# Kernel tuning notes

Measured on AMD Instinct MI355X. Metric: run time of the kernel, lower is better.

## Reference

```python
import jax, jax.numpy as jnp
import numpy as np

EMBED_DIM = 1024
NUM_HEADS = 16
HEAD_DIM = EMBED_DIM // NUM_HEADS
SCALE = HEAD_DIM ** -0.5


def setup_inputs() -> dict:
    key = jax.random.key(0)
    ks = jax.random.split(key, 7)
    B, S, D = 4, 2048, EMBED_DIM
    return {
        "x": jax.random.normal(ks[0], (B, S, D), dtype=jnp.float32),
        "gamma": jnp.ones((D,), dtype=jnp.float32),
        "beta": jnp.zeros((D,), dtype=jnp.float32),
        "w_qkv": jax.random.normal(ks[1], (D, 3 * D), dtype=jnp.float32) * (D ** -0.5),
        "b_qkv": jax.random.normal(ks[2], (3 * D,), dtype=jnp.float32) * 0.02,
        "w_proj": jax.random.normal(ks[3], (D, D), dtype=jnp.float32) * (D ** -0.5),
        "b_proj": jax.random.normal(ks[4], (D,), dtype=jnp.float32) * 0.02,
    }


def reference(x, gamma, beta, w_qkv, b_qkv, w_proj, b_proj):
    B, S, D = x.shape
    # pre-norm LayerNorm (eps=1e-5, torch default)
    mu = jnp.mean(x, axis=-1, keepdims=True)
    var = jnp.mean(jnp.square(x - mu), axis=-1, keepdims=True)
    xn = (x - mu) * jax.lax.rsqrt(var + 1e-5) * gamma + beta
    # fused QKV projection -> (3, B, H, S, hd)
    qkv = (xn @ w_qkv + b_qkv).reshape(B, S, 3, NUM_HEADS, HEAD_DIM)
    qkv = jnp.transpose(qkv, (2, 0, 3, 1, 4))
    q, k, v = qkv[0], qkv[1], qkv[2]
    scores = jnp.einsum("bhqd,bhkd->bhqk", q, k) * SCALE
    attn = jax.nn.softmax(scores, axis=-1)  # dropout p=0 -> no-op
    ctx = jnp.einsum("bhqk,bhkd->bhqd", attn, v)
    ctx = jnp.transpose(ctx, (0, 2, 1, 3)).reshape(B, S, D)
    return ctx @ w_proj + b_proj
```

## Files before the change

kernel.cpp:

```cpp
#include <hip/hip_runtime.h>

typedef unsigned short ushort_t;
typedef __attribute__((ext_vector_type(8))) short bf16x8;
typedef __attribute__((ext_vector_type(4))) float f32x4;
typedef __attribute__((ext_vector_type(16))) float f32x16;
typedef __attribute__((ext_vector_type(2))) __bf16 bf16v2;

#define BN 4
#define SEQ 2048
#define DIM 1024
#define NH 16
#define HDIM 64
#define MROWS (BN*SEQ)
#define QSCALE 0.18033688011112042f

__device__ __forceinline__ float bf2f(ushort_t s){ return __uint_as_float(((unsigned)s) << 16); }
__device__ __forceinline__ ushort_t f2bf(float f){
  unsigned u = __float_as_uint(f);
  u += 0x7fffu + ((u >> 16) & 1u);
  return (ushort_t)(u >> 16);
}
__device__ __forceinline__ unsigned pack2(float a, float b){
  return (unsigned)f2bf(a) | ((unsigned)f2bf(b) << 16);
}

__global__ __launch_bounds__(256) void ln_kernel(const float* __restrict__ x,
                                                 const float* __restrict__ gamma,
                                                 const float* __restrict__ beta,
                                                 ushort_t* __restrict__ xnb)
{
  int row = blockIdx.x;
  int t = threadIdx.x;
  float4 v = ((const float4*)(x + (size_t)row * DIM))[t];
  float s = v.x+v.y+v.z+v.w;
  float ss = v.x*v.x+v.y*v.y+v.z*v.z+v.w*v.w;
  #pragma unroll
  for (int o = 32; o > 0; o >>= 1){ s += __shfl_down(s, o); ss += __shfl_down(ss, o); }
  __shared__ float red[10];
  int wid = t >> 6;
  if ((t & 63) == 0){ red[wid] = s; red[4+wid] = ss; }
  __syncthreads();
  if (t == 0){
    float S0 = red[0]+red[1]+red[2]+red[3];
    float SS = red[4]+red[5]+red[6]+red[7];
    float mu = S0 * (1.f/DIM);
    float var = SS * (1.f/DIM) - mu*mu;
    red[8] = mu; red[9] = rsqrtf(var + 1e-5f);
  }
  __syncthreads();
  float mu = red[8], rstd = red[9];
  float4 g = ((const float4*)gamma)[t];
  float4 b = ((const float4*)beta)[t];
  float f0 = (v.x - mu)*rstd*g.x + b.x;
  float f1 = (v.y - mu)*rstd*g.y + b.y;
  float f2 = (v.z - mu)*rstd*g.z + b.z;
  float f3 = (v.w - mu)*rstd*g.w + b.w;
  *(uint2*)(xnb + (size_t)row*DIM + t*4) = make_uint2(pack2(f0,f1), pack2(f2,f3));
}

__global__ __launch_bounds__(256) void cvt_t(const float* __restrict__ src,
                                             ushort_t* __restrict__ dst,
                                             int K, int N, float qscale)
{
  __shared__ float tile[64][65];
  int k0 = blockIdx.y*64, n0 = blockIdx.x*64;
  float sc = (n0 < 1024) ? qscale : 1.f;
  int t = threadIdx.x;
  int c = (t & 15) * 4, r = t >> 4;
  #pragma unroll
  for (int p = 0; p < 4; p++){
    float4 v = *(const float4*)(src + (size_t)(k0 + r + p*16)*N + n0 + c);
    tile[r+p*16][c]   = v.x; tile[r+p*16][c+1] = v.y;
    tile[r+p*16][c+2] = v.z; tile[r+p*16][c+3] = v.w;
  }
  __syncthreads();
  #pragma unroll
  for (int p = 0; p < 4; p++){
    int nn = r + p*16;
    ushort4 o;
    o.x = f2bf(tile[c+0][nn]*sc); o.y = f2bf(tile[c+1][nn]*sc);
    o.z = f2bf(tile[c+2][nn]*sc); o.w = f2bf(tile[c+3][nn]*sc);
    *(ushort4*)(dst + (size_t)(n0+nn)*K + k0 + c) = o;
  }
}

__global__ __launch_bounds__(256) void vtrans(const ushort_t* __restrict__ V,
                                              ushort_t* __restrict__ vt)
{
  __shared__ ushort_t tile[64][72];
  int bh = blockIdx.x >> 5, sc = blockIdx.x & 31;
  int t = threadIdx.x;
  const ushort_t* src = V + ((size_t)bh*SEQ + sc*64)*HDIM;
  #pragma unroll
  for (int p = 0; p < 2; p++){
    int idx = p*256 + t;
    int r = idx >> 3, c8 = (idx & 7)*8;
    *(uint4*)&tile[r][c8] = *(const uint4*)(src + (size_t)r*HDIM + c8);
  }
  __syncthreads();
  ushort_t* dstp = vt + ((size_t)(bh*32 + sc))*HDIM*64;
  #pragma unroll
  for (int p = 0; p < 2; p++){
    int idx = p*256 + t;
    int d = idx >> 3, c8 = (idx & 7)*8;
    uint4 u;
    u.x = (unsigned)tile[c8+0][d] | ((unsigned)tile[c8+1][d] << 16);
    u.y = (unsigned)tile[c8+2][d] | ((unsigned)tile[c8+3][d] << 16);
    u.z = (unsigned)tile[c8+4][d] | ((unsigned)tile[c8+5][d] << 16);
    u.w = (unsigned)tile[c8+6][d] | ((unsigned)tile[c8+7][d] << 16);
    *(uint4*)(dstp + (size_t)d*64 + c8) = u;
  }
}

template<int MODE, int NCOLS>
__global__ __launch_bounds__(256) void mfma_gemm(
    const ushort_t* __restrict__ A,
    const ushort_t* __restrict__ BT,
    const float* __restrict__ bias,
    void* __restrict__ Cv)
{
  __shared__ __align__(16) unsigned char smem[17408];
  ushort_t (*As)[128][8] = (ushort_t(*)[128][8])smem;
  ushort_t (*Bs)[128][8] = (ushort_t(*)[128][8])(smem + 8192);

  int t = threadIdx.x;
  int lane = t & 63, w = t >> 6;
  int col = lane & 15, quad = lane >> 4;
  int n0 = blockIdx.x * 128, m0 = blockIdx.y * 128;
  int sr = t >> 1, h = t & 1;

  f32x4 acc[4][4];
  #pragma unroll
  for (int i = 0; i < 4; i++)
    #pragma unroll
    for (int j = 0; j < 4; j++) acc[i][j] = (f32x4){0.f,0.f,0.f,0.f};

  int mbase = (w & 1)*64 + col;
  int nbase = (w >> 1)*64 + col;

  for (int k0 = 0; k0 < DIM; k0 += 32){
    const ushort_t* ap = A + (size_t)(m0 + sr)*DIM + k0 + h*16;
    uint4 aa0 = *(const uint4*)ap, aa1 = *(const uint4*)(ap + 8);
    const ushort_t* bp = BT + (size_t)(n0 + sr)*DIM + k0 + h*16;
    uint4 bb0 = *(const uint4*)bp, bb1 = *(const uint4*)(bp + 8);

    __syncthreads();
    *(uint4*)&As[2*h  ][sr][0] = aa0;
    *(uint4*)&As[2*h+1][sr][0] = aa1;
    *(uint4*)&Bs[2*h  ][sr][0] = bb0;
    *(uint4*)&Bs[2*h+1][sr][0] = bb1;
    __syncthreads();

    bf16x8 af[4], bfr[4];
    #pragma unroll
    for (int i = 0; i < 4; i++){
      af[i]  = *(const bf16x8*)&As[quad][mbase + i*16][0];
      bfr[i] = *(const bf16x8*)&Bs[quad][nbase + i*16][0];
    }
    #pragma unroll
    for (int mt = 0; mt < 4; mt++)
      #pragma unroll
      for (int nt = 0; nt < 4; nt++)
        acc[mt][nt] = __builtin_amdgcn_mfma_f32_16x16x32_bf16(af[mt], bfr[nt], acc[mt][nt], 0, 0, 0);
  }

  float bscale = (MODE == 2 && n0 < 1024) ? QSCALE : 1.f;
  float bv[4];
  #pragma unroll
  for (int nt = 0; nt < 4; nt++) bv[nt] = bias[n0 + (w>>1)*64 + nt*16 + col] * bscale;

  if (MODE == 2){
    ushort_t (*Cs)[136] = (ushort_t(*)[136])smem;
    ushort_t* C = (ushort_t*)Cv;
    #pragma unroll
    for (int ph = 0; ph < 2; ph++){
      __syncthreads();
      if ((w & 1) == ph){
        #pragma unroll
        for (int mt = 0; mt < 4; mt++)
          #pragma unroll
          for (int nt = 0; nt < 4; nt++)
            #pragma unroll
            for (int r = 0; r < 4; r++)
              Cs[mt*16 + quad*4 + r][(w>>1)*64 + nt*16 + col] = f2bf(acc[mt][nt][r] + bv[nt]);
      }
      __syncthreads();
      #pragma unroll
      for (int p = 0; p < 4; p++){
        int id = p*256 + t;
        int row = id >> 4, cc = id & 15;
        uint4 u = *(const uint4*)&Cs[row][cc*8];
        int m = m0 + ph*64 + row;
        int n = n0 + cc*8;
        int which = n >> 10, hh = (n >> 6) & 15, d = n & 63;
        int b_ = m >> 11, s_ = m & (SEQ-1);
        *(uint4*)&C[((((size_t)which*BN + b_)*NH + hh)*SEQ + s_)*HDIM + d] = u;
      }
    }
  } else {
    float (*Cf)[132] = (float(*)[132])smem;
    float* C = (float*)Cv;
    #pragma unroll
    for (int ph = 0; ph < 4; ph++){
      __syncthreads();
      if ((w & 1) == (ph >> 1)){
        #pragma unroll
        for (int mi = 0; mi < 2; mi++){
          int mt = (ph & 1)*2 + mi;
          #pragma unroll
          for (int nt = 0; nt < 4; nt++)
            #pragma unroll
            for (int r = 0; r < 4; r++)
              Cf[mi*16 + quad*4 + r][(w>>1)*64 + nt*16 + col] = acc[mt][nt][r] + bv[nt];
        }
      }
      __syncthreads();
      #pragma unroll
      for (int p = 0; p < 4; p++){
        int id = p*256 + t;
        int row = id >> 5, cc = id & 31;
        float4 v = *(const float4*)&Cf[row][cc*4];
        int m = m0 + ph*32 + row;
        *(float4*)(C + (size_t)m*NCOLS + n0 + cc*4) = v;
      }
    }
  }
}

__global__ __launch_bounds__(256) void attn_kernel(const ushort_t* __restrict__ qkv,
                                                   const ushort_t* __restrict__ vtp,
                                                   ushort_t* __restrict__ ctx)
{
  __shared__ __align__(16) unsigned char lds[36864];
  ushort_t (*Ks)[64][8] = (ushort_t(*)[64][8])lds;
  ushort_t (*Vs)[64][8] = (ushort_t(*)[64][8])(lds + 8192);

  int t = threadIdx.x;
  int lane = t & 63, w = t >> 6;
  int m32 = lane & 31, half = lane >> 5;
  int id = blockIdx.x;
  int bh = (id & 7) | ((id >> 7) << 3);
  int qb = (id >> 3) & 15;

  const size_t PL = (size_t)BN * NH * SEQ * HDIM;
  const ushort_t* Qg = qkv + (size_t)bh * (SEQ * HDIM);
  const ushort_t* Kg = Qg + PL;
  const ushort_t* Vt = vtp + (size_t)bh * 32 * (HDIM * 64);
  int qbase = qb*128 + w*32;

  bf16x8 qf[4];
  #pragma unroll
  for (int c = 0; c < 4; c++)
    qf[c] = *(const bf16x8*)(Qg + (size_t)(qbase + m32)*HDIM + c*16 + half*8);

  bf16x8 ones;
  #pragma unroll
  for (int i = 0; i < 8; i++) ones[i] = (short)0x3F80;

  f32x16 accO[2], accL;
  #pragma unroll
  for (int i = 0; i < 2; i++)
    #pragma unroll
    for (int r = 0; r < 16; r++) accO[i][r] = 0.f;
  #pragma unroll
  for (int r = 0; r < 16; r++) accL[r] = 0.f;

  int srow = t >> 2, sch = t & 3;
  const ushort_t* kp0 = Kg + (size_t)srow*HDIM + sch*16;
  const ushort_t* vp0 = Vt + (size_t)srow*64 + sch*16;

  uint4 kr0, kr1, vr0, vr1;
  kr0 = *(const uint4*)kp0;  kr1 = *(const uint4*)(kp0 + 8);
  vr0 = *(const uint4*)vp0;  vr1 = *(const uint4*)(vp0 + 8);

  for (int kt = 0; kt < 32; kt++){
    __syncthreads();
    *(uint4*)&Ks[sch*2  ][srow][0] = kr0;
    *(uint4*)&Ks[sch*2+1][srow][0] = kr1;
    *(uint4*)&Vs[sch*2  ][srow][0] = vr0;
    *(uint4*)&Vs[sch*2+1][srow][0] = vr1;
    __syncthreads();

    if (kt < 31){
      const ushort_t* kp = kp0 + (size_t)(kt+1)*64*HDIM;
      const ushort_t* vp = vp0 + (size_t)(kt+1)*HDIM*64;
      kr0 = *(const uint4*)kp;  kr1 = *(const uint4*)(kp + 8);
      vr0 = *(const uint4*)vp;  vr1 = *(const uint4*)(vp + 8);
    }

    bf16x8 pb[4];
    #pragma unroll
    for (int mt = 0; mt < 2; mt++){
      f32x16 z;
      #pragma unroll
      for (int r = 0; r < 16; r++) z[r] = 0.f;
      #pragma unroll
      for (int c = 0; c < 4; c++){
        bf16x8 af = *(const bf16x8*)&Ks[2*c + half][mt*32 + m32][0];
        z = __builtin_amdgcn_mfma_f32_32x32x16_bf16(af, qf[c], z, 0, 0, 0);
      }
      unsigned u[8];
      #pragma unroll
      for (int i = 0; i < 8; i++){
        float p0 = __builtin_amdgcn_exp2f(z[2*i]);
        float p1 = __builtin_amdgcn_exp2f(z[2*i+1]);
        bf16v2 hh; hh.x = (__bf16)p0; hh.y = (__bf16)p1;
        u[i] = __builtin_bit_cast(unsigned, hh);
      }
      #pragma unroll
      for (int cc = 0; cc < 2; cc++){
        union { uint4 q; bf16x8 b; } cvt;
        cvt.q = make_uint4(u[4*cc+0], u[4*cc+1], u[4*cc+2], u[4*cc+3]);
        pb[mt*2 + cc] = cvt.b;
      }
    }

    #pragma unroll
    for (int kc = 0; kc < 4; kc++)
      accL = __builtin_amdgcn_mfma_f32_32x32x16_bf16(ones, pb[kc], accL, 0, 0, 0);

    #pragma unroll
    for (int kc = 0; kc < 4; kc++){
      #pragma unroll
      for (int md = 0; md < 2; md++){
        int dd = md*32 + m32;
        union { bf16x8 v8; uint2 u2[2]; } vv;
        vv.u2[0] = *(const uint2*)&Vs[2*kc  ][dd][4*half];
        vv.u2[1] = *(const uint2*)&Vs[2*kc+1][dd][4*half];
        accO[md] = __builtin_amdgcn_mfma_f32_32x32x16_bf16(vv.v8, pb[kc], accO[md], 0, 0, 0);
      }
    }
  }

  float inv = 1.f / accL[0];

  ushort_t (*Os)[72] = (ushort_t(*)[72])(lds + 18432 + w*4608);
  #pragma unroll
  for (int md = 0; md < 2; md++)
    #pragma unroll
    for (int g = 0; g < 4; g++){
      int d0 = 8*g + 4*half + 32*md;
      unsigned lo = pack2(accO[md][4*g+0]*inv, accO[md][4*g+1]*inv);
      unsigned hi = pack2(accO[md][4*g+2]*inv, accO[md][4*g+3]*inv);
      *(uint2*)&Os[m32][d0] = make_uint2(lo, hi);
    }

  int b_ = bh >> 4, h_ = bh & 15;
  #pragma unroll
  for (int k = 0; k < 4; k++){
    int row = k*8 + (lane >> 3);
    uint4 u = *(const uint4*)&Os[row][(lane & 7)*8];
    *(uint4*)(ctx + ((size_t)(b_*SEQ + qb*128 + w*32 + row))*DIM + h_*HDIM + (lane & 7)*8) = u;
  }
}

extern "C" void kernel_launch(void* const* d_in, const int* in_sizes, int n_in,
                              void* d_out, int out_size, void* d_ws, size_t ws_size,
                              hipStream_t stream)
{
  const float* x      = (const float*)d_in[0];
  const float* gamma  = (const float*)d_in[1];
  const float* beta   = (const float*)d_in[2];
  const float* w_qkv  = (const float*)d_in[3];
  const float* b_qkv  = (const float*)d_in[4];
  const float* w_proj = (const float*)d_in[5];
  const float* b_proj = (const float*)d_in[6];

  char* ws = (char*)d_ws;
  ushort_t* wqkvT  = (ushort_t*)ws;
  ushort_t* vt     = (ushort_t*)ws;
  ushort_t* wprojT = (ushort_t*)ws;
  ushort_t* qkv    = (ushort_t*)(ws + 16u*1024*1024);
  ushort_t* Vplane = (ushort_t*)(ws + 48u*1024*1024);
  ushort_t* ctx    = (ushort_t*)(ws + 48u*1024*1024);
  ushort_t* xnb    = (ushort_t*)d_out;

  ln_kernel<<<MROWS, 256, 0, stream>>>(x, gamma, beta, xnb);
  cvt_t<<<dim3(3*DIM/64, DIM/64), 256, 0, stream>>>(w_qkv, wqkvT, DIM, 3*DIM, QSCALE);
  mfma_gemm<2, 3*DIM><<<dim3(3*DIM/128, MROWS/128), 256, 0, stream>>>(
      xnb, wqkvT, b_qkv, qkv);
  vtrans<<<BN*NH*(SEQ/64), 256, 0, stream>>>(Vplane, vt);
  attn_kernel<<<BN*NH*(SEQ/128), 256, 0, stream>>>(qkv, vt, ctx);
  cvt_t<<<dim3(DIM/64, DIM/64), 256, 0, stream>>>(w_proj, wprojT, DIM, DIM, 1.f);
  mfma_gemm<0, DIM><<<dim3(DIM/128, MROWS/128), 256, 0, stream>>>(
      ctx, wprojT, b_proj, d_out);
}
```

Baseline: 320.0 us.

## Double attention block to 256 queries with 8 waves and XOR-swizzled K/V LDS

The attention kernel now runs 512 threads per block, so each block covers 256 query rows and every K/V tile staged in LDS serves twice as many waves, halving global K/V traffic per query. The K/V shared-memory layout moves from a chunk-major array to row-major with an XOR swizzle on the 16-byte chunk index to avoid bank conflicts, and each thread now loads one 16-byte chunk per tile instead of two. The row-sum MFMA is interleaved with the PV MFMAs. The trade-off is fewer, larger blocks and more LDS per block (output staging for 8 waves), which may reduce occupancy.

```diff
diff --git a/kernel.cpp b/kernel.cpp
--- a/kernel.cpp
+++ b/kernel.cpp
@@ -227,26 +227,27 @@
   }
 }
 
-__global__ __launch_bounds__(256) void attn_kernel(const ushort_t* __restrict__ qkv,
+__global__ __launch_bounds__(512) void attn_kernel(const ushort_t* __restrict__ qkv,
                                                    const ushort_t* __restrict__ vtp,
                                                    ushort_t* __restrict__ ctx)
 {
-  __shared__ __align__(16) unsigned char lds[36864];
-  ushort_t (*Ks)[64][8] = (ushort_t(*)[64][8])lds;
-  ushort_t (*Vs)[64][8] = (ushort_t(*)[64][8])(lds + 8192);
+  __shared__ __align__(16) unsigned char lds[53248];
+  ushort_t* Ksm = (ushort_t*)lds;
+  ushort_t* Vsm = (ushort_t*)(lds + 8192);
 
   int t = threadIdx.x;
   int lane = t & 63, w = t >> 6;
   int m32 = lane & 31, half = lane >> 5;
+  int r7 = m32 & 7;
   int id = blockIdx.x;
-  int bh = (id & 7) | ((id >> 7) << 3);
-  int qb = (id >> 3) & 15;
+  int bh = (id & 7) | ((id >> 6) << 3);
+  int qb = (id >> 3) & 7;
 
   const size_t PL = (size_t)BN * NH * SEQ * HDIM;
   const ushort_t* Qg = qkv + (size_t)bh * (SEQ * HDIM);
   const ushort_t* Kg = Qg + PL;
   const ushort_t* Vt = vtp + (size_t)bh * 32 * (HDIM * 64);
-  int qbase = qb*128 + w*32;
+  int qbase = qb*256 + w*32;
 
   bf16x8 qf[4];
   #pragma unroll
@@ -265,27 +266,23 @@
   #pragma unroll
   for (int r = 0; r < 16; r++) accL[r] = 0.f;
 
-  int srow = t >> 2, sch = t & 3;
-  const ushort_t* kp0 = Kg + (size_t)srow*HDIM + sch*16;
-  const ushort_t* vp0 = Vt + (size_t)srow*64 + sch*16;
-
-  uint4 kr0, kr1, vr0, vr1;
-  kr0 = *(const uint4*)kp0;  kr1 = *(const uint4*)(kp0 + 8);
-  vr0 = *(const uint4*)vp0;  vr1 = *(const uint4*)(vp0 + 8);
+  int srow = t >> 3, och = t & 7;
+  const ushort_t* kp0 = Kg + (size_t)srow*HDIM + och*8;
+  const ushort_t* vp0 = Vt + (size_t)srow*64 + och*8;
+  int wofs = srow*64 + ((och ^ (srow & 7)) << 3);
+
+  uint4 kr = *(const uint4*)kp0;
+  uint4 vr = *(const uint4*)vp0;
 
   for (int kt = 0; kt < 32; kt++){
     __syncthreads();
-    *(uint4*)&Ks[sch*2  ][srow][0] = kr0;
-    *(uint4*)&Ks[sch*2+1][srow][0] = kr1;
-    *(uint4*)&Vs[sch*2  ][srow][0] = vr0;
-    *(uint4*)&Vs[sch*2+1][srow][0] = vr1;
+    *(uint4*)&Ksm[wofs] = kr;
+    *(uint4*)&Vsm[wofs] = vr;
     __syncthreads();
 
     if (kt < 31){
-      const ushort_t* kp = kp0 + (size_t)(kt+1)*64*HDIM;
-      const ushort_t* vp = vp0 + (size_t)(kt+1)*HDIM*64;
-      kr0 = *(const uint4*)kp;  kr1 = *(const uint4*)(kp + 8);
-      vr0 = *(const uint4*)vp;  vr1 = *(const uint4*)(vp + 8);
+      kr = *(const uint4*)(kp0 + (size_t)(kt+1)*64*HDIM);
+      vr = *(const uint4*)(vp0 + (size_t)(kt+1)*HDIM*64);
     }
 
     bf16x8 pb[4];
@@ -294,9 +291,10 @@
       f32x16 z;
       #pragma unroll
       for (int r = 0; r < 16; r++) z[r] = 0.f;
+      int rowb = (mt*32 + m32) * 64;
       #pragma unroll
       for (int c = 0; c < 4; c++){
-        bf16x8 af = *(const bf16x8*)&Ks[2*c + half][mt*32 + m32][0];
+        bf16x8 af = *(const bf16x8*)&Ksm[rowb + (((2*c + half) ^ r7) << 3)];
         z = __builtin_amdgcn_mfma_f32_32x32x16_bf16(af, qf[c], z, 0, 0, 0);
       }
       unsigned u[8];
@@ -316,17 +314,15 @@
     }
 
     #pragma unroll
-    for (int kc = 0; kc < 4; kc++)
+    for (int kc = 0; kc < 4; kc++){
       accL = __builtin_amdgcn_mfma_f32_32x32x16_bf16(ones, pb[kc], accL, 0, 0, 0);
-
-    #pragma unroll
-    for (int kc = 0; kc < 4; kc++){
       #pragma unroll
       for (int md = 0; md < 2; md++){
         int dd = md*32 + m32;
+        int rowb = dd * 64;
         union { bf16x8 v8; uint2 u2[2]; } vv;
-        vv.u2[0] = *(const uint2*)&Vs[2*kc  ][dd][4*half];
-        vv.u2[1] = *(const uint2*)&Vs[2*kc+1][dd][4*half];
+        vv.u2[0] = *(const uint2*)&Vsm[rowb + (((2*kc  ) ^ r7) << 3) + 4*half];
+        vv.u2[1] = *(const uint2*)&Vsm[rowb + (((2*kc+1) ^ r7) << 3) + 4*half];
         accO[md] = __builtin_amdgcn_mfma_f32_32x32x16_bf16(vv.v8, pb[kc], accO[md], 0, 0, 0);
       }
     }
@@ -334,7 +330,7 @@
 
   float inv = 1.f / accL[0];
 
-  ushort_t (*Os)[72] = (ushort_t(*)[72])(lds + 18432 + w*4608);
+  ushort_t (*Os)[72] = (ushort_t(*)[72])(lds + 16384 + w*4608);
   #pragma unroll
   for (int md = 0; md < 2; md++)
     #pragma unroll
@@ -350,7 +346,7 @@
   for (int k = 0; k < 4; k++){
     int row = k*8 + (lane >> 3);
     uint4 u = *(const uint4*)&Os[row][(lane & 7)*8];
-    *(uint4*)(ctx + ((size_t)(b_*SEQ + qb*128 + w*32 + row))*DIM + h_*HDIM + (lane & 7)*8) = u;
+    *(uint4*)(ctx + ((size_t)(b_*SEQ + qb*256 + w*32 + row))*DIM + h_*HDIM + (lane & 7)*8) = u;
   }
 }
 
@@ -380,7 +376,7 @@
   mfma_gemm<2, 3*DIM><<<dim3(3*DIM/128, MROWS/128), 256, 0, stream>>>(
       xnb, wqkvT, b_qkv, qkv);
   vtrans<<<BN*NH*(SEQ/64), 256, 0, stream>>>(Vplane, vt);
-  attn_kernel<<<BN*NH*(SEQ/128), 256, 0, stream>>>(qkv, vt, ctx);
+  attn_kernel<<<BN*NH*(SEQ/256), 512, 0, stream>>>(qkv, vt, ctx);
   cvt_t<<<dim3(DIM/64, DIM/64), 256, 0, stream>>>(w_proj, wprojT, DIM, DIM, 1.f);
   mfma_gemm<0, DIM><<<dim3(DIM/128, MROWS/128), 256, 0, stream>>>(
       ctx, wprojT, b_proj, d_out);
```

Result: faster. 313.7 us (-2.0%).
